# Kernel tuning notes

Hardware: AMD Instinct MI355X
Metric: run time of the kernel (lower is better)

The kernel has to match this reference:

```python
import jax, jax.numpy as jnp
import numpy as np

N, T, E, B = 50000, 16, 800000, 2000
EMB, ENC, DEC, OUT_LEN = 32, 64, 128, 25
NEG_SLOPE = 0.1
BN_EPS = 1e-5


def lrelu(x):
    return jnp.where(x >= 0, x, NEG_SLOPE * x)


def gru_encode(xs, Wih, Whh, bih, bhh):
    # xs: [T, N, in] -> final hidden [N, H]   (torch GRU gate order: r, z, n)
    H = Whh.shape[1]

    def step(h, x_t):
        gi = x_t @ Wih.T + bih
        gh = h @ Whh.T + bhh
        i_r, i_z, i_n = jnp.split(gi, 3, axis=-1)
        h_r, h_z, h_n = jnp.split(gh, 3, axis=-1)
        r = jax.nn.sigmoid(i_r + h_r)
        z = jax.nn.sigmoid(i_z + h_z)
        n = jnp.tanh(i_n + r * h_n)
        return (1.0 - z) * n + z * h, None

    h0 = jnp.zeros((xs.shape[1], H), xs.dtype)
    hT, _ = jax.lax.scan(step, h0, xs)
    return hT


def lstm_layer(xs, Wih, Whh, bih, bhh):
    # xs: [T, B, in] -> outputs [T, B, H]   (torch LSTM gate order: i, f, g, o)
    H = Whh.shape[1]

    def step(carry, x_t):
        h, c = carry
        g = x_t @ Wih.T + bih + h @ Whh.T + bhh
        i, f, gg, o = jnp.split(g, 4, axis=-1)
        c = jax.nn.sigmoid(f) * c + jax.nn.sigmoid(i) * jnp.tanh(gg)
        h = jax.nn.sigmoid(o) * jnp.tanh(c)
        return (h, c), h

    z0 = jnp.zeros((xs.shape[1], H), xs.dtype)
    _, hs = jax.lax.scan(step, (z0, z0), xs)
    return hs


def cgconv(x, src, dst, edge_attr, Wf, bf, Ws, bs, gamma, beta, mean, var):
    # PyG CGConv: z = [x_i, x_j, e]; msg = sigmoid(lin_f(z)) * softplus(lin_s(z));
    # out = x + BN(scatter_add(msg, i))
    z = jnp.concatenate([x[dst], x[src], edge_attr], axis=-1)  # [E, 2*ENC+2]
    msg = jax.nn.sigmoid(z @ Wf.T + bf) * jax.nn.softplus(z @ Ws.T + bs)
    agg = jax.ops.segment_sum(msg, dst, num_segments=N)  # [N, ENC]
    agg = (agg - mean) * jax.lax.rsqrt(var + BN_EPS) * gamma + beta
    return x + agg


def setup_inputs() -> dict:
    key = jax.random.key(0)
    ks = jax.random.split(key, 32)

    def rn(k, shape, scale=0.1):
        return jax.random.normal(k, shape, jnp.float32) * scale

    inp = {}
    inp["x"] = jax.random.normal(ks[0], (N, T, 2), jnp.float32)
    inp["edge_index"] = jax.random.randint(ks[1], (2, E), 0, N)
    inp["edge_attr"] = jax.random.normal(ks[2], (E, 2), jnp.float32)
    inp["target_index"] = jnp.sort(jax.random.randint(ks[3], (B,), 0, N))
    inp["W_ip"] = rn(ks[4], (EMB, 2)); inp["b_ip"] = jnp.zeros((EMB,), jnp.float32)
    inp["gru_Wih"] = rn(ks[5], (3 * ENC, EMB)); inp["gru_Whh"] = rn(ks[6], (3 * ENC, ENC))
    inp["gru_bih"] = jnp.zeros((3 * ENC,), jnp.float32); inp["gru_bhh"] = jnp.zeros((3 * ENC,), jnp.float32)
    inp["W_dyn"] = rn(ks[7], (ENC, ENC)); inp["b_dyn"] = jnp.zeros((ENC,), jnp.float32)
    Z = 2 * ENC + 2
    for i, base in ((1, 8), (2, 14)):
        inp[f"cg{i}_Wf"] = rn(ks[base], (ENC, Z)); inp[f"cg{i}_bf"] = jnp.zeros((ENC,), jnp.float32)
        inp[f"cg{i}_Ws"] = rn(ks[base + 1], (ENC, Z)); inp[f"cg{i}_bs"] = jnp.zeros((ENC,), jnp.float32)
        inp[f"cg{i}_gamma"] = jnp.ones((ENC,), jnp.float32); inp[f"cg{i}_beta"] = jnp.zeros((ENC,), jnp.float32)
        inp[f"cg{i}_mean"] = jnp.zeros((ENC,), jnp.float32); inp[f"cg{i}_var"] = jnp.ones((ENC,), jnp.float32)
    inp["W_nbrs"] = rn(ks[20], (ENC, ENC)); inp["b_nbrs"] = jnp.zeros((ENC,), jnp.float32)
    inp["lstm0_Wih"] = rn(ks[21], (4 * DEC, 2 * ENC)); inp["lstm0_Whh"] = rn(ks[22], (4 * DEC, DEC))
    inp["lstm0_bih"] = jnp.zeros((4 * DEC,), jnp.float32); inp["lstm0_bhh"] = jnp.zeros((4 * DEC,), jnp.float32)
    inp["lstm1_Wih"] = rn(ks[23], (4 * DEC, DEC)); inp["lstm1_Whh"] = rn(ks[24], (4 * DEC, DEC))
    inp["lstm1_bih"] = jnp.zeros((4 * DEC,), jnp.float32); inp["lstm1_bhh"] = jnp.zeros((4 * DEC,), jnp.float32)
    inp["W_op"] = rn(ks[25], (2, DEC)); inp["b_op"] = jnp.zeros((2,), jnp.float32)
    return inp


def reference(x, edge_index, edge_attr, target_index, W_ip, b_ip,
              gru_Wih, gru_Whh, gru_bih, gru_bhh, W_dyn, b_dyn,
              cg1_Wf, cg1_bf, cg1_Ws, cg1_bs, cg1_gamma, cg1_beta, cg1_mean, cg1_var,
              cg2_Wf, cg2_bf, cg2_Ws, cg2_bs, cg2_gamma, cg2_beta, cg2_mean, cg2_var,
              W_nbrs, b_nbrs,
              lstm0_Wih, lstm0_Whh, lstm0_bih, lstm0_bhh,
              lstm1_Wih, lstm1_Whh, lstm1_bih, lstm1_bhh, W_op, b_op):
    src, dst = edge_index[0], edge_index[1]
    # --- history encoder (GRU) ---
    h = lrelu(x @ W_ip.T + b_ip)                                  # [N, T, EMB]
    hT = gru_encode(h.transpose(1, 0, 2), gru_Wih, gru_Whh, gru_bih, gru_bhh)  # [N, ENC]
    hist = lrelu(lrelu(hT) @ W_dyn.T + b_dyn)                     # [N, ENC]
    # --- CGConv interaction x2 ---
    f = cgconv(hist, src, dst, edge_attr, cg1_Wf, cg1_bf, cg1_Ws, cg1_bs,
               cg1_gamma, cg1_beta, cg1_mean, cg1_var)
    f = cgconv(f, src, dst, edge_attr, cg2_Wf, cg2_bf, cg2_Ws, cg2_bs,
               cg2_gamma, cg2_beta, cg2_mean, cg2_var)
    tar = lrelu(f[target_index] @ W_nbrs.T + b_nbrs)              # [B, ENC]
    enc = jnp.concatenate([hist[target_index], tar], axis=-1)     # [B, 2*ENC]
    # --- LSTM decoder over repeated encoding ---
    xs = jnp.broadcast_to(enc, (OUT_LEN,) + enc.shape)            # [OUT_LEN, B, 2*ENC]
    hs = lstm_layer(xs, lstm0_Wih, lstm0_Whh, lstm0_bih, lstm0_bhh)
    hs = lstm_layer(hs, lstm1_Wih, lstm1_Whh, lstm1_bih, lstm1_bhh)
    fut = hs.transpose(1, 0, 2) @ W_op.T + b_op                   # [B, OUT_LEN, 2]
    return fut
```

## Files before the change

kernel.cpp:

```cpp
#include <hip/hip_runtime.h>
#include <hip/hip_fp16.h>
#include <math.h>

#define NN   50000
#define TT   16
#define EE   800000
#define BB   2000
#define EMBD 32
#define ENC  64
#define DEC  128
#define OUTL 25
#define BN_EPS 1e-5f

typedef short v8s __attribute__((ext_vector_type(8)));
typedef float v4f __attribute__((ext_vector_type(4)));
#define MFMA16(a,b,c) __builtin_amdgcn_mfma_f32_16x16x32_bf16((a),(b),(c),0,0,0)

__device__ __forceinline__ float lrelu(float v){ return v >= 0.f ? v : 0.1f*v; }
__device__ __forceinline__ float fsig(float v){ return __builtin_amdgcn_rcpf(1.f + __expf(-v)); }
__device__ __forceinline__ float ftanh(float v){ return 2.f*__builtin_amdgcn_rcpf(1.f + __expf(-2.f*v)) - 1.f; }
__device__ __forceinline__ float fsoftplus(float v){
    return v > 15.f ? v : __logf(1.f + __expf(v));
}

__device__ __forceinline__ unsigned short f2bf(float f){
    unsigned u = __float_as_uint(f);
    u = u + 0x7FFFu + ((u>>16)&1u);
    return (unsigned short)(u>>16);
}
__device__ __forceinline__ float bf2f(unsigned short s){ return __uint_as_float(((unsigned)s)<<16); }

__device__ __forceinline__ void tsplit(float v, unsigned short& hi, unsigned short& lo){
    unsigned u = __float_as_uint(v);
    hi = (unsigned short)(u >> 16);
    float r = v - __uint_as_float(u & 0xFFFF0000u);
    lo = (unsigned short)(__float_as_uint(r) >> 16);
}

__device__ __forceinline__ v8s as_v8s(int4 v){
    union { int4 i; v8s s; } u; u.i = v; return u.s;
}

__device__ __forceinline__ void cvt8(const float* p, v8s& hi, v8s& lo){
    float4 a0 = *(const float4*)p;
    float4 a1 = *(const float4*)(p+4);
    float av[8] = {a0.x,a0.y,a0.z,a0.w,a1.x,a1.y,a1.z,a1.w};
#pragma unroll
    for (int j=0;j<8;j++){
        unsigned short h = f2bf(av[j]);
        hi[j] = (short)h;
        lo[j] = (short)f2bf(av[j] - bf2f(h));
    }
}
__device__ __forceinline__ void lrelu_resplit(v8s hh, v8s hl, v8s& oh, v8s& ol){
#pragma unroll
    for (int j=0;j<8;j++){
        float v = bf2f((unsigned short)hh[j]) + bf2f((unsigned short)hl[j]);
        float a = lrelu(v);
        unsigned short h = f2bf(a);
        oh[j] = (short)h;
        ol[j] = (short)f2bf(a - bf2f(h));
    }
}

__device__ __forceinline__ void pf_item(const float* W, int K, int KB, int i,
                                        unsigned short* out){
    int l = i & 63, fb = i >> 6;
    int kb = fb % KB, nt = fb / KB;
    int n = nt*16 + (l&15);
    int k0 = kb*32 + ((l>>4)*8);
#pragma unroll
    for (int j=0;j<8;j++) out[i*8+j] = f2bf(W[(size_t)n*K + k0 + j]);
}
__device__ __forceinline__ void phl_item(const float* W, int K, int KB, int i,
                                         unsigned short* hi, unsigned short* lo){
    int l = i & 63, fb = i >> 6;
    int kb = fb % KB, nt = fb / KB;
    int n = nt*16 + (l&15);
    int k0 = kb*32 + ((l>>4)*8);
#pragma unroll
    for (int j=0;j<8;j++){
        float v = W[(size_t)n*K + k0 + j];
        unsigned short h = f2bf(v);
        hi[i*8+j] = h;
        lo[i*8+j] = f2bf(v - bf2f(h));
    }
}
__device__ __forceinline__ void pcat_item(const float* Wa, const float* Wb,
                                          int K1, int K, int KB, int i,
                                          unsigned short* out){
    int l = i & 63, fb = i >> 6;
    int kb = fb % KB, nt = fb / KB;
    int n = nt*16 + (l&15);
    int k0 = kb*32 + ((l>>4)*8);
#pragma unroll
    for (int j=0;j<8;j++){
        int k = k0 + j;
        float v = (k < K1) ? Wa[(size_t)n*K1 + k] : Wb[(size_t)n*(K-K1) + (k-K1)];
        out[i*8+j] = f2bf(v);
    }
}
__device__ __forceinline__ void pproj_item(const float* Wf, const float* Ws, int i,
                                           unsigned short* hi, unsigned short* lo){
    int l = i & 63, fb = i >> 6;
    int kb = fb & 1, nt = fb >> 1;
    int n = nt*16 + (l&15);
    int d = n >> 6, c = n & 63;
    const float* W = (d < 2) ? Wf : Ws;
    int k0 = (d&1)*64 + kb*32 + ((l>>4)*8);
#pragma unroll
    for (int j=0;j<8;j++){
        float v = W[c*130 + k0 + j];
        unsigned short h = f2bf(v);
        hi[i*8+j] = h;
        lo[i*8+j] = f2bf(v - bf2f(h));
    }
}

__global__ void pack_all(
    const float* __restrict__ gWih, const float* __restrict__ gWhh,
    const float* __restrict__ Wdyn,
    const float* __restrict__ l0Whh, const float* __restrict__ l1Wih,
    const float* __restrict__ l1Whh, const float* __restrict__ l0Wih,
    const float* __restrict__ c1Wf, const float* __restrict__ c1Ws,
    const float* __restrict__ c2Wf, const float* __restrict__ c2Ws,
    unsigned short* __restrict__ pWih, unsigned short* __restrict__ pWhh,
    unsigned short* __restrict__ pWdyn,
    unsigned short* __restrict__ B0h, unsigned short* __restrict__ B1h,
    unsigned short* __restrict__ P1h, unsigned short* __restrict__ P1l,
    unsigned short* __restrict__ P2h, unsigned short* __restrict__ P2l,
    unsigned short* __restrict__ GIh, unsigned short* __restrict__ GIl,
    int* __restrict__ cnt, int* __restrict__ gtot)
{
    int i = blockIdx.x*256 + threadIdx.x;
    if (i < 768){ pf_item(gWih, 32, 1, i, pWih); return; }   i -= 768;
    if (i < 1536){ pf_item(gWhh, 64, 2, i, pWhh); return; }  i -= 1536;
    if (i < 512){ pf_item(Wdyn, 64, 2, i, pWdyn); return; }  i -= 512;
    if (i < 8192){ pcat_item(l0Whh, l0Whh, 128, 128, 4, i, B0h); return; } i -= 8192;
    if (i < 16384){ pcat_item(l1Wih, l1Whh, 128, 256, 8, i, B1h); return; } i -= 16384;
    if (i < 2048){ pproj_item(c1Wf, c1Ws, i, P1h, P1l); return; } i -= 2048;
    if (i < 2048){ pproj_item(c2Wf, c2Ws, i, P2h, P2l); return; } i -= 2048;
    if (i < 8192){ phl_item(l0Wih, 128, 4, i, GIh, GIl); return; } i -= 8192;
    if (i < NN){ cnt[i] = 0; return; } i -= NN;
    if (i < 1){ gtot[0] = 0; return; }
}
#define PACK_TOTAL (768+1536+512+8192+16384+2048+2048+8192+NN+1)

__global__ __launch_bounds__(256) void encoder_mfma(
    const float* __restrict__ x,
    const float* __restrict__ Wip, const float* __restrict__ bip,
    const unsigned short* __restrict__ pWih,
    const unsigned short* __restrict__ pWhh,
    const float* __restrict__ bih, const float* __restrict__ bhh,
    const unsigned short* __restrict__ pWdyn,
    const float* __restrict__ bdyn,
    float* __restrict__ hist)
{
    __shared__ unsigned short efh[4*512], efl[4*512];
    __shared__ unsigned short hfh[2][1024], hfl[2][1024];
    const int tid = threadIdx.x;
    const int l   = tid & 63;
    const int w   = tid >> 6;
    const int ln  = l & 15, q = l >> 4;
    const int blk = blockIdx.x;
    const int rsw = ((l>>1)&7)<<3;

    for (int i = tid; i < 1024; i += 256){
        hfh[0][i]=0; hfl[0][i]=0; hfh[1][i]=0; hfl[1][i]=0;
    }

    const int k0 = tid & 31;
    const int mb = tid >> 5;
    const float ew0 = Wip[2*k0], ew1 = Wip[2*k0+1], ebk = bip[k0];
    const int ebase = (k0>>3)*128 + (k0&7);
    const float2* xr0 = (const float2*)(x + (size_t)(blk*16 + 2*mb    )*32);
    const float2* xr1 = (const float2*)(x + (size_t)(blk*16 + 2*mb + 1)*32);

    const int c = w*16 + ln;
    const float bR  = bih[c]       + bhh[c];
    const float bZ  = bih[64 + c]  + bhh[64 + c];
    const float bNI = bih[128 + c];
    const float bNH = bhh[128 + c];
    float hprev[4] = {0.f,0.f,0.f,0.f};

    const v8s* FIH = (const v8s*)pWih;
    const v8s* FHH = (const v8s*)pWhh;
    const v8s* FDY = (const v8s*)pWdyn;
    const int wbase = (c>>5)*512 + (16*((c&31)>>3))*8 + (c&7);
    __syncthreads();

    int p = 0;
#pragma unroll 1
    for (int tb = 0; tb < 4; tb++){
#pragma unroll
        for (int ts = 0; ts < 4; ts++){
            int t = tb*4 + ts;
            float2 xv0 = xr0[t], xv1 = xr1[t];
            float e0 = lrelu(ew0*xv0.x + ew1*xv0.y + ebk);
            float e1 = lrelu(ew0*xv1.x + ew1*xv1.y + ebk);
            unsigned short h_, l_;
            tsplit(e0, h_, l_);
            efh[ts*512 + ebase + (2*mb  )*8] = h_;
            efl[ts*512 + ebase + (2*mb  )*8] = l_;
            tsplit(e1, h_, l_);
            efh[ts*512 + ebase + (2*mb+1)*8] = h_;
            efl[ts*512 + ebase + (2*mb+1)*8] = l_;
        }
        __syncthreads();
#pragma unroll 1
        for (int ts = 0; ts < 4; ts++){
            v8s eh  = *(const v8s*)&efh[ts*512 + l*8];
            v8s el  = *(const v8s*)&efl[ts*512 + l*8];
            v8s h0h = *(const v8s*)&hfh[p][(l*8) ^ rsw];
            v8s h0l = *(const v8s*)&hfl[p][(l*8) ^ rsw];
            v8s h1h = *(const v8s*)&hfh[p][512 + ((l*8) ^ rsw)];
            v8s h1l = *(const v8s*)&hfl[p][512 + ((l*8) ^ rsw)];

            v4f aR = {bR,bR,bR,bR};
            v4f aZ = {bZ,bZ,bZ,bZ};
            v4f aNI= {bNI,bNI,bNI,bNI};
            v4f aNH= {bNH,bNH,bNH,bNH};
            v8s b;
            b = FIH[(w   )*64 + l];    aR = MFMA16(eh,b,aR);  aR = MFMA16(el,b,aR);
            b = FHH[(w*2+0)*64+l];     aR = MFMA16(h0h,b,aR); aR = MFMA16(h0l,b,aR);
            b = FHH[(w*2+1)*64+l];     aR = MFMA16(h1h,b,aR); aR = MFMA16(h1l,b,aR);
            b = FIH[(4+w )*64 + l];    aZ = MFMA16(eh,b,aZ);  aZ = MFMA16(el,b,aZ);
            b = FHH[((4+w)*2+0)*64+l]; aZ = MFMA16(h0h,b,aZ); aZ = MFMA16(h0l,b,aZ);
            b = FHH[((4+w)*2+1)*64+l]; aZ = MFMA16(h1h,b,aZ); aZ = MFMA16(h1l,b,aZ);
            b = FIH[(8+w )*64 + l];    aNI= MFMA16(eh,b,aNI); aNI= MFMA16(el,b,aNI);
            b = FHH[((8+w)*2+0)*64+l]; aNH= MFMA16(h0h,b,aNH);aNH= MFMA16(h0l,b,aNH);
            b = FHH[((8+w)*2+1)*64+l]; aNH= MFMA16(h1h,b,aNH);aNH= MFMA16(h1l,b,aNH);

#pragma unroll
            for (int i = 0; i < 4; i++){
                float r_ = fsig(aR[i]);
                float z_ = fsig(aZ[i]);
                float nn_ = ftanh(aNI[i] + r_*aNH[i]);
                float hn = nn_ + z_*(hprev[i] - nn_);
                hprev[i] = hn;
                int row = q*4 + i;
                int off = (wbase + row*8) ^ ((((row)>>1)&7)<<3);
                unsigned short hh_, hl_;
                tsplit(hn, hh_, hl_);
                hfh[1-p][off] = hh_;
                hfl[1-p][off] = hl_;
            }
            __syncthreads();
            p ^= 1;
        }
    }
    {
        v8s a0h,a0l,a1h,a1l;
        lrelu_resplit(*(const v8s*)&hfh[p][(l*8) ^ rsw],
                      *(const v8s*)&hfl[p][(l*8) ^ rsw],       a0h, a0l);
        lrelu_resplit(*(const v8s*)&hfh[p][512 + ((l*8) ^ rsw)],
                      *(const v8s*)&hfl[p][512 + ((l*8) ^ rsw)], a1h, a1l);
        const int nt = w;
        float bb = bdyn[nt*16 + ln];
        v4f acc = {bb,bb,bb,bb};
        v8s b;
        b = FDY[(nt*2+0)*64 + l]; acc = MFMA16(a0h,b,acc); acc = MFMA16(a0l,b,acc);
        b = FDY[(nt*2+1)*64 + l]; acc = MFMA16(a1h,b,acc); acc = MFMA16(a1l,b,acc);
#pragma unroll
        for (int i = 0; i < 4; i++){
            hist[(size_t)(blk*16 + q*4 + i)*64 + nt*16 + ln] = lrelu(acc[i]);
        }
    }
}

#define PROJ_ACC(NT, ACC) { \
    v8s bh0_ = FH[((NT)*2+0)*64 + l], bl0_ = FL[((NT)*2+0)*64 + l]; \
    v8s bh1_ = FH[((NT)*2+1)*64 + l], bl1_ = FL[((NT)*2+1)*64 + l]; \
    ACC = MFMA16(ah0,bh0_,ACC); ACC = MFMA16(al0,bh0_,ACC); ACC = MFMA16(ah0,bl0_,ACC); \
    ACC = MFMA16(ah1,bh1_,ACC); ACC = MFMA16(al1,bh1_,ACC); ACC = MFMA16(ah1,bl1_,ACC); }

__global__ __launch_bounds__(256) void proj_mfma(
    const float* __restrict__ xin,
    const unsigned short* __restrict__ Bh, const unsigned short* __restrict__ Bl,
    float* __restrict__ Af, float* __restrict__ As,
    unsigned* __restrict__ BP)
{
    __shared__ float sx[64*68];
    const int tid = threadIdx.x;
    const int l = tid & 63;
    const int w = tid >> 6;
    const int ln = l & 15, q = l >> 4;
    const int n0 = blockIdx.x*64;

    for (int i=tid;i<64*16;i+=256){
        int nn = i>>4, f4 = i&15;
        float4 v = {0.f,0.f,0.f,0.f};
        if (n0+nn < NN) v = ((const float4*)(xin + (size_t)(n0+nn)*64))[f4];
        *(float4*)&sx[nn*68 + f4*4] = v;
    }
    __syncthreads();

    v8s ah0,al0,ah1,al1;
    cvt8(&sx[(w*16+ln)*68 +      q*8], ah0, al0);
    cvt8(&sx[(w*16+ln)*68 + 32 + q*8], ah1, al1);

    const v8s* FH = (const v8s*)Bh;
    const v8s* FL = (const v8s*)Bl;
#pragma unroll 1
    for (int c3=0; c3<4; c3++){
        v4f aA = {0.f,0.f,0.f,0.f};
        v4f aS = aA, aF = aA, aB = aA;
        PROJ_ACC(c3,      aA);
        PROJ_ACC(8 + c3,  aS);
        PROJ_ACC(4 + c3,  aF);
        PROJ_ACC(12 + c3, aB);
        int col = c3*16 + ln;
#pragma unroll
        for (int i=0;i<4;i++){
            int node = n0 + w*16 + q*4 + i;
            if (node < NN){
                Af[(size_t)node*64 + col] = aA[i];
                As[(size_t)node*64 + col] = aS[i];
                unsigned pf = __half_as_ushort(__float2half(aF[i]));
                unsigned ps = __half_as_ushort(__float2half(aB[i]));
                BP[(size_t)node*64 + col] = pf | (ps << 16);
            }
        }
    }
}

__global__ void count_kernel(const int* __restrict__ ei, int* __restrict__ cnt){
    int e = blockIdx.x*256 + threadIdx.x;
    if (e < EE) atomicAdd(&cnt[ei[EE+e]], 1);
}

__global__ void alloc_kernel(const int* __restrict__ cnt, int* __restrict__ gtot,
                             int* __restrict__ off, int* __restrict__ cur){
    int n = blockIdx.x*256 + threadIdx.x;
    if (n >= NN) return;
    int c = cnt[n];
    int s = atomicAdd(gtot, c);
    off[n] = s;
    cur[n] = s;
}

__global__ void scatter_kernel(const int* __restrict__ ei, const float* __restrict__ ea,
                               int* __restrict__ cur, int2* __restrict__ recS){
    int e = blockIdx.x*256 + threadIdx.x;
    if (e >= EE) return;
    int d = ei[EE+e];
    int p = atomicAdd(&cur[d], 1);
    unsigned e0 = __half_as_ushort(__float2half(ea[2*(size_t)e]));
    unsigned e1 = __half_as_ushort(__float2half(ea[2*(size_t)e+1]));
    int2 r;
    r.x = ei[e];
    r.y = (int)(e0 | (e1 << 16));
    recS[p] = r;
}

__global__ __launch_bounds__(256) void cg_agg(
    const float* __restrict__ xin,
    const int2* __restrict__ recS,
    const int* __restrict__ off, const int* __restrict__ cnt,
    const float* __restrict__ Wf, const float* __restrict__ bf,
    const float* __restrict__ Ws, const float* __restrict__ bs,
    const float* __restrict__ Af, const float* __restrict__ As,
    const unsigned* __restrict__ BP,
    const float* __restrict__ gamma, const float* __restrict__ beta,
    const float* __restrict__ mean, const float* __restrict__ var,
    float* __restrict__ outp)
{
    const int tid = threadIdx.x;
    const int c = tid & 63, wid = tid >> 6;
    const int n = blockIdx.x*4 + wid;
    if (n >= NN) return;

    const float wf0 = Wf[c*130+128], wf1 = Wf[c*130+129], bfc = bf[c];
    const float ws0 = Ws[c*130+128], ws1 = Ws[c*130+129], bsc = bs[c];
    const float afd = Af[(size_t)n*64+c] + bfc, asd = As[(size_t)n*64+c] + bsc;
    const unsigned* BPc = BP + c;

    float acc = 0.f;
    int i = off[n];
    const int i1 = i + cnt[n];
#pragma unroll 1
    for (; i+1 < i1; i += 2){
        int2 r0 = recS[i], r1 = recS[i+1];
        unsigned ea0 = (unsigned)r0.y, ea1 = (unsigned)r1.y;
        float e00 = __half2float(__ushort_as_half((unsigned short)(ea0 & 0xFFFFu)));
        float e01 = __half2float(__ushort_as_half((unsigned short)(ea0 >> 16)));
        float e10 = __half2float(__ushort_as_half((unsigned short)(ea1 & 0xFFFFu)));
        float e11 = __half2float(__ushort_as_half((unsigned short)(ea1 >> 16)));
        unsigned pv0 = BPc[(size_t)r0.x*64];
        unsigned pv1 = BPc[(size_t)r1.x*64];
        float bf0v = __half2float(__ushort_as_half((unsigned short)(pv0 & 0xFFFFu)));
        float bs0v = __half2float(__ushort_as_half((unsigned short)(pv0 >> 16)));
        float bf1v = __half2float(__ushort_as_half((unsigned short)(pv1 & 0xFFFFu)));
        float bs1v = __half2float(__ushort_as_half((unsigned short)(pv1 >> 16)));
        float gf0 = afd + bf0v + wf0*e00 + wf1*e01;
        float gs0 = asd + bs0v + ws0*e00 + ws1*e01;
        float gf1 = afd + bf1v + wf0*e10 + wf1*e11;
        float gs1 = asd + bs1v + ws0*e10 + ws1*e11;
        acc += fsig(gf0)*fsoftplus(gs0);
        acc += fsig(gf1)*fsoftplus(gs1);
    }
    if (i < i1){
        int2 r0 = recS[i];
        unsigned ea0 = (unsigned)r0.y;
        float e00 = __half2float(__ushort_as_half((unsigned short)(ea0 & 0xFFFFu)));
        float e01 = __half2float(__ushort_as_half((unsigned short)(ea0 >> 16)));
        unsigned pv0 = BPc[(size_t)r0.x*64];
        float bf0v = __half2float(__ushort_as_half((unsigned short)(pv0 & 0xFFFFu)));
        float bs0v = __half2float(__ushort_as_half((unsigned short)(pv0 >> 16)));
        float gf = afd + bf0v + wf0*e00 + wf1*e01;
        float gs = asd + bs0v + ws0*e00 + ws1*e01;
        acc += fsig(gf)*fsoftplus(gs);
    }
    float bn = (acc - mean[c])*rsqrtf(var[c]+BN_EPS)*gamma[c] + beta[c];
    outp[(size_t)n*64+c] = xin[(size_t)n*64+c] + bn;
}

__global__ __launch_bounds__(256) void target_kernel(
    const float* __restrict__ hist, const float* __restrict__ f2,
    const int* __restrict__ tgt,
    const float* __restrict__ Wn, const float* __restrict__ bn_,
    float* __restrict__ enc)
{
    const int tid=threadIdx.x;
    const int c = tid&63, q = tid>>6;
    const int b = blockIdx.x*4 + q;
    if (b>=BB) return;
    const int n = tgt[b];
    float a = bn_[c];
#pragma unroll
    for (int k=0;k<ENC;k++) a += Wn[c*64+k]*f2[(size_t)n*64+k];
    enc[(size_t)b*128 + 64 + c] = lrelu(a);
    enc[(size_t)b*128 + c]      = hist[(size_t)n*64+c];
}

__global__ __launch_bounds__(512) void gi0_mfma(
    const float* __restrict__ enc,
    const unsigned short* __restrict__ GIh, const unsigned short* __restrict__ GIl,
    const float* __restrict__ bih0, const float* __restrict__ bhh0,
    float* __restrict__ gi0)
{
    __shared__ float senc[16*132];
    const int tid = threadIdx.x;
    const int l = tid & 63;
    const int w = tid >> 6;
    const int ln = l & 15, q = l >> 4;
    const int b0 = blockIdx.x*16;

    for (int i=tid;i<16*32;i+=512){
        int row = i>>5, f4 = i&31;
        *(float4*)&senc[row*132 + f4*4] = ((const float4*)(enc + (size_t)(b0+row)*128))[f4];
    }
    __syncthreads();

    v8s ah[4], al[4];
#pragma unroll
    for (int kb=0;kb<4;kb++) cvt8(&senc[ln*132 + kb*32 + q*8], ah[kb], al[kb]);

    const v8s* FH = (const v8s*)GIh;
    const v8s* FL = (const v8s*)GIl;
#pragma unroll
    for (int u=0;u<4;u++){
        int nt = w*4 + u;
        int col = nt*16 + ln;
        float bb = bih0[col] + bhh0[col];
        v4f acc = {bb,bb,bb,bb};
#pragma unroll
        for (int kb=0;kb<4;kb++){
            v8s bh = FH[(nt*4+kb)*64 + l];
            v8s bl = FL[(nt*4+kb)*64 + l];
            acc = MFMA16(ah[kb],bh,acc); acc = MFMA16(al[kb],bh,acc); acc = MFMA16(ah[kb],bl,acc);
        }
#pragma unroll
        for (int i=0;i<4;i++)
            gi0[(size_t)(b0 + q*4 + i)*512 + col] = acc[i];
    }
}

#define LMB 16
__global__ __launch_bounds__(512)
__attribute__((amdgpu_waves_per_eu(2,2)))
void lstm_mfma(
    const float* __restrict__ gi0,
    const unsigned short* __restrict__ B0h,
    const unsigned short* __restrict__ B1h,
    const float* __restrict__ bih1, const float* __restrict__ bhh1,
    float* __restrict__ h1buf)
{
    __shared__ int4 sW0[32*4*64];
    __shared__ unsigned short h0hi[2][4*512], h0lo[2][4*512];
    __shared__ unsigned short h1hi[2][4*512], h1lo[2][4*512];
    const int tid = threadIdx.x;
    const int l = tid & 63;
    const int w = tid >> 6;
    const int c = l & 15;
    const int q = l >> 4;
    const int j = w*16 + c;
    const int b0 = blockIdx.x*LMB;
    const int lsw = ((l>>1)&7)<<3;

    {
        const int4* F0 = (const int4*)B0h;
        for (int i=tid;i<32*4*64;i+=512) sW0[i] = F0[i];
    }
    for (int i=tid;i<4*512;i+=512){
        h0hi[0][i]=0; h0lo[0][i]=0; h0hi[1][i]=0; h0lo[1][i]=0;
        h1hi[0][i]=0; h1lo[0][i]=0; h1hi[1][i]=0; h1lo[1][i]=0;
    }

    int4 W1r[32];
    {
        const int4* F1 = (const int4*)B1h;
#pragma unroll
        for (int g=0;g<4;g++)
#pragma unroll
            for (int kb=0;kb<8;kb++) W1r[g*8+kb] = F1[((g*8+w)*8 + kb)*64 + l];
#pragma unroll
        for (int i=0;i<32;i++)
            asm volatile("" : "+v"(W1r[i].x), "+v"(W1r[i].y), "+v"(W1r[i].z), "+v"(W1r[i].w));
    }

    float rgi[4][4];
#pragma unroll
    for (int g=0;g<4;g++)
#pragma unroll
        for (int i=0;i<4;i++)
            rgi[g][i] = gi0[(size_t)(b0 + q*4 + i)*512 + g*128 + j];

    float b1[4];
#pragma unroll
    for (int g=0;g<4;g++) b1[g] = bih1[g*128+j] + bhh1[g*128+j];
    float c0[4] = {0,0,0,0}, c1[4] = {0,0,0,0};
    const int kbw = j>>5, qw = (j>>3)&3, jw = j&7;
    __syncthreads();

    int p = 0;
#pragma unroll 1
    for (int t=0;t<OUTL;t++){
        v4f aH[4], aL[4];
#pragma unroll
        for (int g=0;g<4;g++){
            v4f t4 = {rgi[g][0], rgi[g][1], rgi[g][2], rgi[g][3]};
            aH[g] = t4;
            v4f z = {0.f,0.f,0.f,0.f};
            aL[g] = z;
        }
#pragma unroll
        for (int kb=0;kb<4;kb++){
            v8s ah = *(const v8s*)&h0hi[p][kb*512 + ((l*8) ^ lsw)];
            v8s al = *(const v8s*)&h0lo[p][kb*512 + ((l*8) ^ lsw)];
#pragma unroll
            for (int g=0;g<4;g++){
                v8s bfr = as_v8s(sW0[((g*8+w)*4 + kb)*64 + l]);
                aH[g] = MFMA16(ah, bfr, aH[g]);
                aL[g] = MFMA16(al, bfr, aL[g]);
            }
        }
#pragma unroll
        for (int i=0;i<4;i++){
            float gi_ = aH[0][i]+aL[0][i], gf_ = aH[1][i]+aL[1][i];
            float gg_ = aH[2][i]+aL[2][i], go_ = aH[3][i]+aL[3][i];
            c0[i] = fsig(gf_)*c0[i] + fsig(gi_)*ftanh(gg_);
            float hn = fsig(go_)*ftanh(c0[i]);
            int row = q*4 + i;
            int off = (kbw*512 + (qw*16 + row)*8 + jw) ^ (((row>>1)&7)<<3);
            unsigned short h = f2bf(hn);
            h0hi[1-p][off] = h;
            h0lo[1-p][off] = f2bf(hn - bf2f(h));
        }
        __syncthreads();

        v4f bH[4], bL[4];
#pragma unroll
        for (int g=0;g<4;g++){
            v4f t4={b1[g],b1[g],b1[g],b1[g]}; bH[g]=t4;
            v4f z={0.f,0.f,0.f,0.f}; bL[g]=z;
        }
#pragma unroll
        for (int kb=0;kb<8;kb++){
            const unsigned short* hb = (kb<4) ? h0hi[1-p] : h1hi[p];
            const unsigned short* lb = (kb<4) ? h0lo[1-p] : h1lo[p];
            int kk = kb & 3;
            v8s ah = *(const v8s*)&hb[kk*512 + ((l*8) ^ lsw)];
            v8s al = *(const v8s*)&lb[kk*512 + ((l*8) ^ lsw)];
#pragma unroll
            for (int g=0;g<4;g++){
                bH[g] = MFMA16(ah, as_v8s(W1r[g*8+kb]), bH[g]);
                bL[g] = MFMA16(al, as_v8s(W1r[g*8+kb]), bL[g]);
            }
        }
        float h1new[4];
#pragma unroll
        for (int i=0;i<4;i++){
            float gi_ = bH[0][i]+bL[0][i], gf_ = bH[1][i]+bL[1][i];
            float gg_ = bH[2][i]+bL[2][i], go_ = bH[3][i]+bL[3][i];
            c1[i] = fsig(gf_)*c1[i] + fsig(gi_)*ftanh(gg_);
            h1new[i] = fsig(go_)*ftanh(c1[i]);
            int row = q*4 + i;
            int off = (kbw*512 + (qw*16 + row)*8 + jw) ^ (((row>>1)&7)<<3);
            unsigned short h = f2bf(h1new[i]);
            h1hi[1-p][off] = h;
            h1lo[1-p][off] = f2bf(h1new[i] - bf2f(h));
        }

#pragma unroll
        for (int i=0;i<4;i++){
            h1buf[((size_t)(b0 + q*4 + i)*OUTL + t)*DEC + j] = h1new[i];
        }
        p ^= 1;
    }
}

__global__ __launch_bounds__(256) void out_proj(
    const float* __restrict__ h1buf,
    const float* __restrict__ Wop, const float* __restrict__ bop,
    float* __restrict__ outp)
{
    int idx = blockIdx.x*256 + threadIdx.x;
    if (idx >= BB*OUTL) return;
    const float4* hp = (const float4*)(h1buf + (size_t)idx*DEC);
    const float4* w0 = (const float4*)Wop;
    const float4* w1 = (const float4*)(Wop + DEC);
    float a0 = 0.f, a1 = 0.f;
#pragma unroll
    for (int k=0;k<32;k++){
        float4 h = hp[k], x0 = w0[k], x1 = w1[k];
        a0 += h.x*x0.x + h.y*x0.y + h.z*x0.z + h.w*x0.w;
        a1 += h.x*x1.x + h.y*x1.y + h.z*x1.z + h.w*x1.w;
    }
    outp[(size_t)idx*2    ] = a0 + bop[0];
    outp[(size_t)idx*2 + 1] = a1 + bop[1];
}

extern "C" void kernel_launch(void* const* d_in, const int* in_sizes, int n_in,
                              void* d_out, int out_size, void* d_ws, size_t ws_size,
                              hipStream_t stream)
{
    const float* x    = (const float*)d_in[0];
    const int*   ei   = (const int*)d_in[1];
    const float* ea   = (const float*)d_in[2];
    const int*   tgt  = (const int*)d_in[3];
    const float* Wip  = (const float*)d_in[4];
    const float* bip  = (const float*)d_in[5];
    const float* gWih = (const float*)d_in[6];
    const float* gWhh = (const float*)d_in[7];
    const float* gbih = (const float*)d_in[8];
    const float* gbhh = (const float*)d_in[9];
    const float* Wdyn = (const float*)d_in[10];
    const float* bdyn = (const float*)d_in[11];
    const float* c1Wf=(const float*)d_in[12]; const float* c1bf=(const float*)d_in[13];
    const float* c1Ws=(const float*)d_in[14]; const float* c1bs=(const float*)d_in[15];
    const float* c1g =(const float*)d_in[16]; const float* c1b =(const float*)d_in[17];
    const float* c1m =(const float*)d_in[18]; const float* c1v =(const float*)d_in[19];
    const float* c2Wf=(const float*)d_in[20]; const float* c2bf=(const float*)d_in[21];
    const float* c2Ws=(const float*)d_in[22]; const float* c2bs=(const float*)d_in[23];
    const float* c2g =(const float*)d_in[24]; const float* c2b =(const float*)d_in[25];
    const float* c2m =(const float*)d_in[26]; const float* c2v =(const float*)d_in[27];
    const float* Wn  =(const float*)d_in[28]; const float* bn_ =(const float*)d_in[29];
    const float* l0Wih=(const float*)d_in[30]; const float* l0Whh=(const float*)d_in[31];
    const float* l0bih=(const float*)d_in[32]; const float* l0bhh=(const float*)d_in[33];
    const float* l1Wih=(const float*)d_in[34]; const float* l1Whh=(const float*)d_in[35];
    const float* l1bih=(const float*)d_in[36]; const float* l1bhh=(const float*)d_in[37];
    const float* Wop =(const float*)d_in[38]; const float* bop=(const float*)d_in[39];

    float* ws = (float*)d_ws;
    size_t o = 0;
    float* hist = ws + o; o += (size_t)NN*ENC;
    float* f1   = ws + o; o += (size_t)NN*ENC;
    float* f2   = ws + o; o += (size_t)NN*ENC;
    float* Af   = ws + o; o += (size_t)NN*ENC;
    float* Bfs  = ws + o; o += (size_t)NN*ENC;
    float* As   = ws + o; o += (size_t)NN*ENC;
    float* enc  = ws + o; o += (size_t)BB*2*ENC;
    float* gi0  = ws + o; o += (size_t)BB*4*DEC;
    unsigned short* pWih  = (unsigned short*)(ws + o); o += (size_t)12*64*8/2;
    unsigned short* pWhh  = (unsigned short*)(ws + o); o += (size_t)24*64*8/2;
    unsigned short* pWdyn = (unsigned short*)(ws + o); o += (size_t)8*64*8/2;
    unsigned short* B0h = (unsigned short*)(ws + o); o += (size_t)32*4*64*8/2;
    unsigned short* B1h = (unsigned short*)(ws + o); o += (size_t)32*8*64*8/2;
    unsigned short* P1h = (unsigned short*)(ws + o); o += (size_t)2048*8/2;
    unsigned short* P1l = (unsigned short*)(ws + o); o += (size_t)2048*8/2;
    unsigned short* P2h = (unsigned short*)(ws + o); o += (size_t)2048*8/2;
    unsigned short* P2l = (unsigned short*)(ws + o); o += (size_t)2048*8/2;
    unsigned short* GIh = (unsigned short*)(ws + o); o += (size_t)8192*8/2;
    unsigned short* GIl = (unsigned short*)(ws + o); o += (size_t)8192*8/2;
    int* cnt    = (int*)(ws + o); o += NN;
    int* offv   = (int*)(ws + o); o += NN+1;
    int* curv   = (int*)(ws + o); o += NN;
    int* gtot   = (int*)(ws + o); o += 1;
    o = (o + 3) & ~(size_t)3;
    int2* recS  = (int2*)(ws + o); o += (size_t)2*EE;

    unsigned* BP = (unsigned*)Bfs;

    float* h1buf = Af;

    pack_all<<<(PACK_TOTAL+255)/256, 256, 0, stream>>>(
        gWih, gWhh, Wdyn, l0Whh, l1Wih, l1Whh, l0Wih,
        c1Wf, c1Ws, c2Wf, c2Ws,
        pWih, pWhh, pWdyn, B0h, B1h, P1h, P1l, P2h, P2l, GIh, GIl, cnt, gtot);

    count_kernel<<<(EE+255)/256, 256, 0, stream>>>(ei, cnt);
    alloc_kernel<<<(NN+255)/256, 256, 0, stream>>>(cnt, gtot, offv, curv);
    scatter_kernel<<<(EE+255)/256, 256, 0, stream>>>(ei, ea, curv, recS);

    encoder_mfma<<<NN/16, 256, 0, stream>>>(x, Wip, bip, pWih, pWhh, gbih, gbhh, pWdyn, bdyn, hist);

    proj_mfma<<<(NN+63)/64, 256, 0, stream>>>(hist, P1h, P1l, Af, As, BP);
    cg_agg<<<(NN+3)/4, 256, 0, stream>>>(hist, recS, offv, cnt,
                                         c1Wf,c1bf,c1Ws,c1bs, Af, As, BP,
                                         c1g,c1b,c1m,c1v, f1);

    proj_mfma<<<(NN+63)/64, 256, 0, stream>>>(f1, P2h, P2l, Af, As, BP);
    cg_agg<<<(NN+3)/4, 256, 0, stream>>>(f1, recS, offv, cnt,
                                         c2Wf,c2bf,c2Ws,c2bs, Af, As, BP,
                                         c2g,c2b,c2m,c2v, f2);

    target_kernel<<<(BB+3)/4, 256, 0, stream>>>(hist, f2, tgt, Wn, bn_, enc);

    gi0_mfma<<<BB/16, 512, 0, stream>>>(enc, GIh, GIl, l0bih, l0bhh, gi0);

    lstm_mfma<<<BB/LMB, 512, 0, stream>>>(gi0, B0h, B1h,
                                          l1bih, l1bhh, h1buf);

    out_proj<<<(BB*OUTL+255)/256, 256, 0, stream>>>(h1buf, Wop, bop, (float*)d_out);
}
```

Baseline: 573.2 us.

## Fuse edge degree counting into encoder launch and unroll edge aggregation by four

The separate edge-count kernel goes away. Its atomic degree counting now runs in extra blocks appended to the GRU encoder grid, so the memory-bound counting overlaps with the compute-bound encoder and one launch is dropped. The CGConv aggregation loop is also refactored into a helper and unrolled by four instead of two, giving more independent gathers in flight. The cost is extra register pressure in cg_agg, and block scheduling order may delay the count blocks behind the encoder blocks.

```diff
diff --git a/kernel.cpp b/kernel.cpp
--- a/kernel.cpp
+++ b/kernel.cpp
@@ -146,6 +146,8 @@
 }
 #define PACK_TOTAL (768+1536+512+8192+16384+2048+2048+8192+NN+1)
 
+#define ENCB (NN/16)
+#define CNTB ((EE+255)/256)
 __global__ __launch_bounds__(256) void encoder_mfma(
     const float* __restrict__ x,
     const float* __restrict__ Wip, const float* __restrict__ bip,
@@ -154,11 +156,19 @@
     const float* __restrict__ bih, const float* __restrict__ bhh,
     const unsigned short* __restrict__ pWdyn,
     const float* __restrict__ bdyn,
-    float* __restrict__ hist)
+    float* __restrict__ hist,
+    const int* __restrict__ ei, int* __restrict__ cnt)
 {
     __shared__ unsigned short efh[4*512], efl[4*512];
     __shared__ unsigned short hfh[2][1024], hfl[2][1024];
     const int tid = threadIdx.x;
+
+    if (blockIdx.x >= ENCB){
+        int e = (blockIdx.x - ENCB)*256 + tid;
+        if (e < EE) atomicAdd(&cnt[ei[EE+e]], 1);
+        return;
+    }
+
     const int l   = tid & 63;
     const int w   = tid >> 6;
     const int ln  = l & 15, q = l >> 4;
@@ -324,11 +334,6 @@
     }
 }
 
-__global__ void count_kernel(const int* __restrict__ ei, int* __restrict__ cnt){
-    int e = blockIdx.x*256 + threadIdx.x;
-    if (e < EE) atomicAdd(&cnt[ei[EE+e]], 1);
-}
-
 __global__ void alloc_kernel(const int* __restrict__ cnt, int* __restrict__ gtot,
                              int* __restrict__ off, int* __restrict__ cur){
     int n = blockIdx.x*256 + threadIdx.x;
@@ -353,6 +358,21 @@
     recS[p] = r;
 }
 
+__device__ __forceinline__ float edge_term(
+    int2 r, const unsigned* BPc,
+    float afd, float asd, float wf0, float wf1, float ws0, float ws1)
+{
+    unsigned ea = (unsigned)r.y;
+    float e0 = __half2float(__ushort_as_half((unsigned short)(ea & 0xFFFFu)));
+    float e1 = __half2float(__ushort_as_half((unsigned short)(ea >> 16)));
+    unsigned pv = BPc[(size_t)r.x*64];
+    float bfv = __half2float(__ushort_as_half((unsigned short)(pv & 0xFFFFu)));
+    float bsv = __half2float(__ushort_as_half((unsigned short)(pv >> 16)));
+    float gf = afd + bfv + wf0*e0 + wf1*e1;
+    float gs = asd + bsv + ws0*e0 + ws1*e1;
+    return fsig(gf)*fsoftplus(gs);
+}
+
 __global__ __launch_bounds__(256) void cg_agg(
     const float* __restrict__ xin,
     const int2* __restrict__ recS,
@@ -379,37 +399,16 @@
     int i = off[n];
     const int i1 = i + cnt[n];
 #pragma unroll 1
-    for (; i+1 < i1; i += 2){
-        int2 r0 = recS[i], r1 = recS[i+1];
-        unsigned ea0 = (unsigned)r0.y, ea1 = (unsigned)r1.y;
-        float e00 = __half2float(__ushort_as_half((unsigned short)(ea0 & 0xFFFFu)));
-        float e01 = __half2float(__ushort_as_half((unsigned short)(ea0 >> 16)));
-        float e10 = __half2float(__ushort_as_half((unsigned short)(ea1 & 0xFFFFu)));
-        float e11 = __half2float(__ushort_as_half((unsigned short)(ea1 >> 16)));
-        unsigned pv0 = BPc[(size_t)r0.x*64];
-        unsigned pv1 = BPc[(size_t)r1.x*64];
-        float bf0v = __half2float(__ushort_as_half((unsigned short)(pv0 & 0xFFFFu)));
-        float bs0v = __half2float(__ushort_as_half((unsigned short)(pv0 >> 16)));
-        float bf1v = __half2float(__ushort_as_half((unsigned short)(pv1 & 0xFFFFu)));
-        float bs1v = __half2float(__ushort_as_half((unsigned short)(pv1 >> 16)));
-        float gf0 = afd + bf0v + wf0*e00 + wf1*e01;
-        float gs0 = asd + bs0v + ws0*e00 + ws1*e01;
-        float gf1 = afd + bf1v + wf0*e10 + wf1*e11;
-        float gs1 = asd + bs1v + ws0*e10 + ws1*e11;
-        acc += fsig(gf0)*fsoftplus(gs0);
-        acc += fsig(gf1)*fsoftplus(gs1);
-    }
-    if (i < i1){
-        int2 r0 = recS[i];
-        unsigned ea0 = (unsigned)r0.y;
-        float e00 = __half2float(__ushort_as_half((unsigned short)(ea0 & 0xFFFFu)));
-        float e01 = __half2float(__ushort_as_half((unsigned short)(ea0 >> 16)));
-        unsigned pv0 = BPc[(size_t)r0.x*64];
-        float bf0v = __half2float(__ushort_as_half((unsigned short)(pv0 & 0xFFFFu)));
-        float bs0v = __half2float(__ushort_as_half((unsigned short)(pv0 >> 16)));
-        float gf = afd + bf0v + wf0*e00 + wf1*e01;
-        float gs = asd + bs0v + ws0*e00 + ws1*e01;
-        acc += fsig(gf)*fsoftplus(gs);
+    for (; i+3 < i1; i += 4){
+        int2 r0 = recS[i], r1 = recS[i+1], r2 = recS[i+2], r3 = recS[i+3];
+        acc += edge_term(r0, BPc, afd, asd, wf0, wf1, ws0, ws1);
+        acc += edge_term(r1, BPc, afd, asd, wf0, wf1, ws0, ws1);
+        acc += edge_term(r2, BPc, afd, asd, wf0, wf1, ws0, ws1);
+        acc += edge_term(r3, BPc, afd, asd, wf0, wf1, ws0, ws1);
+    }
+#pragma unroll 1
+    for (; i < i1; i++){
+        acc += edge_term(recS[i], BPc, afd, asd, wf0, wf1, ws0, ws1);
     }
     float bn = (acc - mean[c])*rsqrtf(var[c]+BN_EPS)*gamma[c] + beta[c];
     outp[(size_t)n*64+c] = xin[(size_t)n*64+c] + bn;
@@ -699,11 +698,11 @@
         c1Wf, c1Ws, c2Wf, c2Ws,
         pWih, pWhh, pWdyn, B0h, B1h, P1h, P1l, P2h, P2l, GIh, GIl, cnt, gtot);
 
-    count_kernel<<<(EE+255)/256, 256, 0, stream>>>(ei, cnt);
+    encoder_mfma<<<ENCB + CNTB, 256, 0, stream>>>(
+        x, Wip, bip, pWih, pWhh, gbih, gbhh, pWdyn, bdyn, hist, ei, cnt);
+
     alloc_kernel<<<(NN+255)/256, 256, 0, stream>>>(cnt, gtot, offv, curv);
     scatter_kernel<<<(EE+255)/256, 256, 0, stream>>>(ei, ea, curv, recS);
-
-    encoder_mfma<<<NN/16, 256, 0, stream>>>(x, Wip, bip, pWih, pWhh, gbih, gbhh, pWdyn, bdyn, hist);
 
     proj_mfma<<<(NN+63)/64, 256, 0, stream>>>(hist, P1h, P1l, Af, As, BP);
     cg_agg<<<(NN+3)/4, 256, 0, stream>>>(hist, recS, offv, cnt,
```

New measurement: 540.8 us. 1.06x faster.
